# Performance work log

Hardware: AMD Instinct MI355X
Metric: run time of the kernel (lower is better)

The kernel has to match this reference:

```python
import jax, jax.numpy as jnp
import numpy as np

NHEAD, HD, ITERS = 8, 32, 6


def _layernorm(x, g, b, eps=1e-5):
    mu = jnp.mean(x, axis=-1, keepdims=True)
    var = jnp.mean((x - mu) ** 2, axis=-1, keepdims=True)
    return g * (x - mu) / jnp.sqrt(var + eps) + b


def _msa1(x, ax, WQ, bQ, WK, bK, WV, bV, WO, bO):
    # ring (sliding-window, size 3) attention + relay node as 4th key/value
    B, L, H = x.shape
    q = (x @ WQ + bQ).reshape(B, L, NHEAD, HD)
    k = (x @ WK + bK).reshape(B, L, NHEAD, HD)
    ak = (ax @ WK + bK).reshape(B, 1, NHEAD, 1, HD)   # relay key
    av = (ax @ WV + bV).reshape(B, 1, NHEAD, 1, HD)   # relay value
    padk = jnp.pad(k, ((0, 0), (1, 1), (0, 0), (0, 0)))
    wins = jnp.stack([padk[:, t:L + t] for t in range(3)], axis=3)  # [B,L,nh,3,hd]
    ak_b = jnp.broadcast_to(ak, (B, L, NHEAD, 1, HD))
    av_b = jnp.broadcast_to(av, (B, L, NHEAD, 1, HD))
    keys = jnp.concatenate([ak_b, wins], axis=3)   # [B,L,nh,4,hd]
    # NOTE: faithful to source bug: window VALUES come from k (pad_v = F.pad(k,...))
    vals = jnp.concatenate([av_b, wins], axis=3)
    scores = jnp.einsum('blnd,blnkd->blnk', q, keys) / np.sqrt(HD).astype(np.float32)
    alphas = jax.nn.softmax(scores, axis=-1)
    att = jnp.einsum('blnk,blnkd->blnd', alphas, vals).reshape(B, L, NHEAD * HD)
    return att @ WO + bO


def _msa2(x, y, WQ, bQ, WK, bK, WV, bV, WO, bO):
    # relay attends over [relay; nodes]; mask arg is ignored in the original
    B, L1, H = y.shape
    q = (x @ WQ + bQ).reshape(B, NHEAD, HD)
    k = (y @ WK + bK).reshape(B, L1, NHEAD, HD)
    v = (y @ WV + bV).reshape(B, L1, NHEAD, HD)
    scores = jnp.einsum('bnd,blnd->bnl', q, k) / np.sqrt(HD).astype(np.float32)
    alphas = jax.nn.softmax(scores, axis=-1)
    att = jnp.einsum('bnl,blnd->bnd', alphas, v).reshape(B, NHEAD * HD)
    return att @ WO + bO


def setup_inputs() -> dict:
    key = jax.random.key(0)
    ks = jax.random.split(key, 32)
    B, L, H, V, E, I = 32, 512, 256, 32000, 300, 6

    def rn(k, shape, s=0.05):
        return jax.random.normal(k, shape, jnp.float32) * s

    inp = {
        'data': jax.random.randint(ks[0], (B, L), 0, V),
        'emb': rn(ks[1], (V, E), 0.1),
        'emb_fc_W': rn(ks[2], (E, H)),
        'emb_fc_b': jnp.zeros((H,), jnp.float32),
        'pos_emb': rn(ks[3], (1000, H), 0.02),
        'ln_g': jnp.ones((I, H), jnp.float32),
        'ln_b': jnp.zeros((I, H), jnp.float32),
    }
    names = ['r_WQ', 'r_WK', 'r_WV', 'r_WO', 's_WQ', 's_WK', 's_WV', 's_WO']
    for j, n in enumerate(names):
        inp[n] = rn(ks[4 + j], (I, H, H))
        inp[n.replace('W', 'b')] = rn(ks[12 + j], (I, H), 0.01)
    return inp


def reference(data, emb, emb_fc_W, emb_fc_b, pos_emb, ln_g, ln_b,
              r_WQ, r_bQ, r_WK, r_bK, r_WV, r_bV, r_WO, r_bO,
              s_WQ, s_bQ, s_WK, s_bK, s_WV, s_bV, s_WO, s_bO):
    B, L = data.shape
    mask = (data == 1)
    e = emb[data]                                  # [B,L,nemb]
    P = pos_emb[:L][None]                          # [1,L,H]
    x0 = e @ emb_fc_W + emb_fc_b + P               # [B,L,H]
    nodes = x0
    relay = jnp.mean(x0, axis=1)                   # [B,H]
    for i in range(ITERS):
        ax = relay
        n_ln = _layernorm(nodes, ln_g[i], ln_b[i])
        nodes = nodes + jax.nn.leaky_relu(
            _msa1(n_ln, ax, r_WQ[i], r_bQ[i], r_WK[i], r_bK[i],
                  r_WV[i], r_bV[i], r_WO[i], r_bO[i]))
        y = jnp.concatenate([relay[:, None, :], nodes], axis=1)
        relay = jax.nn.leaky_relu(
            _msa2(relay, y, s_WQ[i], s_bQ[i], s_WK[i], s_bK[i],
                  s_WV[i], s_bV[i], s_WO[i], s_bO[i]))
        nodes = jnp.where(mask[:, :, None], 0.0, nodes)
    rep = 0.5 * jnp.max(nodes, axis=1) + 0.5 * relay
    return rep
```

## Files before the change

kernel.cpp:

```cpp
#include <hip/hip_runtime.h>
#include <stdint.h>

typedef __bf16 bf16x8 __attribute__((ext_vector_type(8)));
typedef unsigned short ushort8 __attribute__((ext_vector_type(8)));
typedef float floatx4 __attribute__((ext_vector_type(4)));

__device__ __forceinline__ unsigned short f2b(float f) {
    unsigned int u = __builtin_bit_cast(unsigned int, f);
    u += 0x7fffu + ((u >> 16) & 1u);
    return (unsigned short)(u >> 16);
}
__device__ __forceinline__ float b2f(unsigned short u) {
    union { unsigned int i; float f; } x; x.i = ((unsigned int)u) << 16; return x.f;
}
__device__ __forceinline__ void gl_lds16(const unsigned short* g, unsigned short* l) {
    __builtin_amdgcn_global_load_lds(
        (const __attribute__((address_space(1))) unsigned int*)g,
        (__attribute__((address_space(3))) unsigned int*)l, 16, 0, 0);
}

#define SCALE_QK 0.17677669529663687f

__global__ void transpose_many(const float* __restrict__ w0,
                               const float* __restrict__ w1,
                               const float* __restrict__ w2,
                               const float* __restrict__ w3,
                               const float* __restrict__ w4,
                               unsigned short* __restrict__ out) {
    int m = blockIdx.y;
    int fam = m / 6, it = m % 6;
    const float* src =
        (fam == 0 ? w0 : fam == 1 ? w1 : fam == 2 ? w2 : fam == 3 ? w3 : w4) + it * 65536;
    int e = blockIdx.x * 256 + threadIdx.x;
    int n = e >> 8, k = e & 255;
    out[(size_t)(it * 5 + fam) * 65536 + e] = f2b(src[k * 256 + n]);
}

__global__ void transpose_emb(const float* __restrict__ W,
                              unsigned short* __restrict__ out) {
    int e = blockIdx.x * 256 + threadIdx.x;
    int n = e / 320, k = e % 320;
    out[e] = (k < 300) ? f2b(W[k * 256 + n]) : (unsigned short)0;
}

__global__ void gather_emb(const int* __restrict__ data,
                           const float* __restrict__ emb,
                           unsigned short* __restrict__ apad) {
    int row = blockIdx.x;
    int tok = data[row];
    const float* er = emb + (size_t)tok * 300;
    for (int c = threadIdx.x; c < 320; c += 256)
        apad[(size_t)row * 320 + c] = (c < 300) ? f2b(er[c]) : (unsigned short)0;
}

template <int EPI, int KDIM>
__global__ __launch_bounds__(256) void gemm_k(const unsigned short* __restrict__ A,
                                              const unsigned short* __restrict__ Bt,
                                              const float* __restrict__ bias0,
                                              const float* __restrict__ bias1,
                                              float* __restrict__ outF,
                                              unsigned short* __restrict__ outB0,
                                              unsigned short* __restrict__ outB1,
                                              const float* __restrict__ pos,
                                              const int* __restrict__ dmask,
                                              int applyMask) {
    constexpr int G = KDIM / 8;
    __shared__ unsigned short Asm[64 * KDIM];
    __shared__ unsigned short Bsm[64 * KDIM];
    const int tid = threadIdx.x;
    const int wave = tid >> 6, lane = tid & 63;
    const int wm = (wave >> 1) * 32, wn = (wave & 1) * 32;
    const int quad = lane >> 4, l16 = lane & 15;
    const int rowBase = blockIdx.x * 64, colBase = blockIdx.y * 64;

    {
        const unsigned short* gbA = A + (size_t)(rowBase + wave * 16) * KDIM;
        const unsigned short* gbB = Bt + (size_t)(colBase + wave * 16) * KDIM;
        unsigned short* lbA = Asm + wave * 16 * KDIM;
        unsigned short* lbB = Bsm + wave * 16 * KDIM;
#pragma unroll
        for (int c = 0; c < G / 4; c++) {
            int gi = c * 64 + lane;
            int rl = gi / G, sl = gi - rl * G;
            int sg = sl ^ (rl & 7);
            gl_lds16(gbA + rl * KDIM + sg * 8, lbA + gi * 8);
            gl_lds16(gbB + rl * KDIM + sg * 8, lbB + gi * 8);
        }
    }
    __syncthreads();

    floatx4 acc[2][2] = {};
    const int mr0 = wm + l16, mr1 = wm + 16 + l16;
    const int nr0 = wn + l16, nr1 = wn + 16 + l16;
#pragma unroll
    for (int ks = 0; ks < KDIM / 32; ks++) {
        int g = ks * 4 + quad;
        bf16x8 af0 = __builtin_bit_cast(bf16x8, *(const ushort8*)&Asm[mr0 * KDIM + ((g ^ (mr0 & 7)) * 8)]);
        bf16x8 af1 = __builtin_bit_cast(bf16x8, *(const ushort8*)&Asm[mr1 * KDIM + ((g ^ (mr1 & 7)) * 8)]);
        bf16x8 bf0 = __builtin_bit_cast(bf16x8, *(const ushort8*)&Bsm[nr0 * KDIM + ((g ^ (nr0 & 7)) * 8)]);
        bf16x8 bf1 = __builtin_bit_cast(bf16x8, *(const ushort8*)&Bsm[nr1 * KDIM + ((g ^ (nr1 & 7)) * 8)]);
        acc[0][0] = __builtin_amdgcn_mfma_f32_16x16x32_bf16(af0, bf0, acc[0][0], 0, 0, 0);
        acc[0][1] = __builtin_amdgcn_mfma_f32_16x16x32_bf16(af0, bf1, acc[0][1], 0, 0, 0);
        acc[1][0] = __builtin_amdgcn_mfma_f32_16x16x32_bf16(af1, bf0, acc[1][0], 0, 0, 0);
        acc[1][1] = __builtin_amdgcn_mfma_f32_16x16x32_bf16(af1, bf1, acc[1][1], 0, 0, 0);
    }
    const int group = colBase >> 8;
    const float* bias = (EPI == 0 && group) ? bias1 : bias0;
    unsigned short* obf = (EPI == 0 && group) ? outB1 : outB0;
#pragma unroll
    for (int tm = 0; tm < 2; tm++) {
#pragma unroll
        for (int tn = 0; tn < 2; tn++) {
            int col = colBase + wn + tn * 16 + l16;
            int lc = col & 255;
            float bv = bias[lc];
#pragma unroll
            for (int r = 0; r < 4; r++) {
                int row = rowBase + wm + tm * 16 + quad * 4 + r;
                float c = acc[tm][tn][r] + bv;
                size_t o = (size_t)row * 256 + lc;
                if (EPI == 0) {
                    obf[o] = f2b(c);
                } else if (EPI == 1) {
                    float v = c > 0.f ? c : 0.01f * c;
                    float base = outF[o];
                    if (applyMask && dmask[row] == 1) base = 0.f;
                    float rr = base + v;
                    outF[o] = rr;
                    outB0[o] = f2b(rr);
                } else {
                    outF[o] = c + pos[(row & 511) * 256 + lc];
                }
            }
        }
    }
}

__global__ void mean_part(const float* __restrict__ nodes, float* __restrict__ part) {
    int b = blockIdx.x, c = blockIdx.y, h = threadIdx.x;
    const float* p = nodes + ((size_t)b * 512 + c * 32) * 256 + h;
    float s = 0.f;
    for (int l = 0; l < 32; l++) s += p[l * 256];
    part[(b * 16 + c) * 256 + h] = s;
}
__global__ void mean_comb(const float* __restrict__ part, float* __restrict__ relay) {
    int b = blockIdx.x, h = threadIdx.x;
    float s = 0.f;
    for (int c = 0; c < 16; c++) s += part[(b * 16 + c) * 256 + h];
    relay[b * 256 + h] = s * (1.f / 512.f);
}

__global__ __launch_bounds__(256) void ln_k(const float* __restrict__ nodes,
                                            const float* __restrict__ g,
                                            const float* __restrict__ bb,
                                            unsigned short* __restrict__ out,
                                            const int* __restrict__ dmask,
                                            int applyMask) {
    __shared__ float red[8];
    int row = blockIdx.x, t = threadIdx.x;
    int wv = t >> 6, ln_ = t & 63;
    float x = nodes[(size_t)row * 256 + t];
    if (applyMask && dmask[row] == 1) x = 0.f;
    float s = x;
#pragma unroll
    for (int o = 32; o; o >>= 1) s += __shfl_xor(s, o);
    if (ln_ == 0) red[wv] = s;
    __syncthreads();
    float mu = (red[0] + red[1] + red[2] + red[3]) * (1.f / 256.f);
    float d = x - mu;
    float v = d * d;
#pragma unroll
    for (int o = 32; o; o >>= 1) v += __shfl_xor(v, o);
    if (ln_ == 0) red[4 + wv] = v;
    __syncthreads();
    float var = (red[4] + red[5] + red[6] + red[7]) * (1.f / 256.f);
    float inv = rsqrtf(var + 1e-5f);
    out[(size_t)row * 256 + t] = f2b(g[t] * d * inv + bb[t]);
}

__global__ void relay5(const float* __restrict__ relay,
                       const float* __restrict__ rWK, const float* __restrict__ rbK,
                       const float* __restrict__ rWV, const float* __restrict__ rbV,
                       const float* __restrict__ sWQ, const float* __restrict__ sbQ,
                       const float* __restrict__ sWK, const float* __restrict__ sbK,
                       const float* __restrict__ sWV, const float* __restrict__ sbV,
                       float* __restrict__ AK, float* __restrict__ AV,
                       float* __restrict__ Q2, float* __restrict__ RK2, float* __restrict__ RV2) {
    __shared__ float r[256];
    int b = blockIdx.x, fam = blockIdx.y, t = threadIdx.x;
    r[t] = relay[b * 256 + t];
    __syncthreads();
    const float* W; const float* bi; float* o;
    switch (fam) {
        case 0: W = rWK; bi = rbK; o = AK; break;
        case 1: W = rWV; bi = rbV; o = AV; break;
        case 2: W = sWQ; bi = sbQ; o = Q2; break;
        case 3: W = sWK; bi = sbK; o = RK2; break;
        default: W = sWV; bi = sbV; o = RV2; break;
    }
    float s = 0.f;
    for (int e = 0; e < 256; e++) s += r[e] * W[e * 256 + t];
    o[b * 256 + t] = s + bi[t];
}

__global__ __launch_bounds__(256) void attn1_k(const unsigned short* __restrict__ q,
                                               const unsigned short* __restrict__ k,
                                               const float* __restrict__ ak,
                                               const float* __restrict__ av,
                                               unsigned short* __restrict__ att) {
    int tid = threadIdx.x;
    int row = blockIdx.x * 4 + (tid >> 6);
    int b = row >> 9, l = row & 511;
    int t = tid & 63;
    size_t o = (size_t)row * 256 + t * 4;
    ushort4 z4; z4.x = z4.y = z4.z = z4.w = 0;
    ushort4 q4 = *(const ushort4*)(q + o);
    ushort4 k04 = *(const ushort4*)(k + o);
    ushort4 km4 = (l > 0) ? *(const ushort4*)(k + o - 256) : z4;
    ushort4 kp4 = (l < 511) ? *(const ushort4*)(k + o + 256) : z4;
    float4 akv = *(const float4*)(ak + b * 256 + t * 4);
    float4 avv = *(const float4*)(av + b * 256 + t * 4);
    float qv0 = b2f(q4.x), qv1 = b2f(q4.y), qv2 = b2f(q4.z), qv3 = b2f(q4.w);
    float k00 = b2f(k04.x), k01 = b2f(k04.y), k02 = b2f(k04.z), k03 = b2f(k04.w);
    float km0 = b2f(km4.x), km1 = b2f(km4.y), km2 = b2f(km4.z), km3 = b2f(km4.w);
    float kp0 = b2f(kp4.x), kp1 = b2f(kp4.y), kp2 = b2f(kp4.z), kp3 = b2f(kp4.w);
    float s0 = qv0 * akv.x + qv1 * akv.y + qv2 * akv.z + qv3 * akv.w;
    float s1 = qv0 * km0 + qv1 * km1 + qv2 * km2 + qv3 * km3;
    float s2 = qv0 * k00 + qv1 * k01 + qv2 * k02 + qv3 * k03;
    float s3 = qv0 * kp0 + qv1 * kp1 + qv2 * kp2 + qv3 * kp3;
#pragma unroll
    for (int off = 4; off; off >>= 1) {
        s0 += __shfl_xor(s0, off);
        s1 += __shfl_xor(s1, off);
        s2 += __shfl_xor(s2, off);
        s3 += __shfl_xor(s3, off);
    }
    s0 *= SCALE_QK; s1 *= SCALE_QK; s2 *= SCALE_QK; s3 *= SCALE_QK;
    float m = fmaxf(fmaxf(s0, s1), fmaxf(s2, s3));
    float e0 = __expf(s0 - m), e1 = __expf(s1 - m), e2 = __expf(s2 - m), e3 = __expf(s3 - m);
    float iZ = 1.f / (e0 + e1 + e2 + e3);
    ushort4 r4;
    r4.x = f2b((e0 * avv.x + e1 * km0 + e2 * k00 + e3 * kp0) * iZ);
    r4.y = f2b((e0 * avv.y + e1 * km1 + e2 * k01 + e3 * kp1) * iZ);
    r4.z = f2b((e0 * avv.z + e1 * km2 + e2 * k02 + e3 * kp2) * iZ);
    r4.w = f2b((e0 * avv.w + e1 * km3 + e2 * k03 + e3 * kp3) * iZ);
    *(ushort4*)(att + o) = r4;
}

__global__ __launch_bounds__(256) void attn2_k(const float* __restrict__ q2,
                                               const unsigned short* __restrict__ k2,
                                               const unsigned short* __restrict__ v2,
                                               const float* __restrict__ rk2,
                                               const float* __restrict__ rv2,
                                               float* __restrict__ att2) {
    __shared__ float sc[513];
    __shared__ float qs[32];
    __shared__ float red[16];
    __shared__ float red2[256];
    int bn = blockIdx.x;
    int b = bn >> 3, n = bn & 7;
    int t = threadIdx.x;
    if (t < 32) qs[t] = q2[b * 256 + n * 32 + t];
    __syncthreads();
    float lmax = -1e30f;
    for (int li = t; li < 513; li += 256) {
        float d = 0.f;
        if (li == 0) {
            const float* kr = rk2 + b * 256 + n * 32;
#pragma unroll 8
            for (int j = 0; j < 32; j++) d += qs[j] * kr[j];
        } else {
            const unsigned short* kr = k2 + ((size_t)(b * 512 + li - 1) * 256 + n * 32);
#pragma unroll 8
            for (int j = 0; j < 32; j++) d += qs[j] * b2f(kr[j]);
        }
        d *= SCALE_QK;
        sc[li] = d;
        lmax = fmaxf(lmax, d);
    }
#pragma unroll
    for (int o = 32; o; o >>= 1) lmax = fmaxf(lmax, __shfl_xor(lmax, o));
    if ((t & 63) == 0) red[t >> 6] = lmax;
    __syncthreads();
    float m = fmaxf(fmaxf(red[0], red[1]), fmaxf(red[2], red[3]));
    float lsum = 0.f;
    for (int li = t; li < 513; li += 256) {
        float e = __expf(sc[li] - m);
        sc[li] = e;
        lsum += e;
    }
#pragma unroll
    for (int o = 32; o; o >>= 1) lsum += __shfl_xor(lsum, o);
    if ((t & 63) == 0) red[8 + (t >> 6)] = lsum;
    __syncthreads();
    float Z = red[8] + red[9] + red[10] + red[11];
    int d_ = t & 31, g_ = t >> 5;
    float acc = 0.f;
    for (int li = g_; li < 513; li += 8) {
        if (li == 0) {
            acc += sc[0] * rv2[b * 256 + n * 32 + d_];
        } else {
            acc += sc[li] * b2f(v2[(size_t)(b * 512 + li - 1) * 256 + n * 32 + d_]);
        }
    }
    red2[t] = acc;
    __syncthreads();
    if (t < 32) {
        float s = 0.f;
        for (int g = 0; g < 8; g++) s += red2[g * 32 + t];
        att2[b * 256 + n * 32 + t] = s / Z;
    }
}

__global__ void relay_out2(const float* __restrict__ att2,
                           const float* __restrict__ WO, const float* __restrict__ bO,
                           float* __restrict__ relay) {
    __shared__ float r[256];
    int b = blockIdx.x, t = threadIdx.x;
    r[t] = att2[b * 256 + t];
    __syncthreads();
    float s = 0.f;
    for (int e = 0; e < 256; e++) s += r[e] * WO[e * 256 + t];
    s += bO[t];
    relay[b * 256 + t] = s > 0.f ? s : 0.01f * s;
}

__global__ void rep_part(const float* __restrict__ nodes, const int* __restrict__ dmask,
                         float* __restrict__ part) {
    int b = blockIdx.x, c = blockIdx.y, h = threadIdx.x;
    const float* p = nodes + ((size_t)b * 512 + c * 32) * 256 + h;
    const int* dd = dmask + b * 512 + c * 32;
    float m = -1e30f;
    for (int l = 0; l < 32; l++) {
        float v = (dd[l] == 1) ? 0.f : p[l * 256];
        m = fmaxf(m, v);
    }
    part[(b * 16 + c) * 256 + h] = m;
}
__global__ void rep_comb(const float* __restrict__ part, const float* __restrict__ relay,
                         float* __restrict__ out) {
    int b = blockIdx.x, h = threadIdx.x;
    float m = -1e30f;
    for (int c = 0; c < 16; c++) m = fmaxf(m, part[(b * 16 + c) * 256 + h]);
    out[b * 256 + h] = 0.5f * m + 0.5f * relay[b * 256 + h];
}

extern "C" void kernel_launch(void* const* d_in, const int* in_sizes, int n_in,
                              void* d_out, int out_size, void* d_ws, size_t ws_size,
                              hipStream_t stream) {
    const int* data = (const int*)d_in[0];
    const float* emb = (const float*)d_in[1];
    const float* emb_fc_W = (const float*)d_in[2];
    const float* emb_fc_b = (const float*)d_in[3];
    const float* pos_emb = (const float*)d_in[4];
    const float* ln_g = (const float*)d_in[5];
    const float* ln_b = (const float*)d_in[6];
    const float* r_WQ = (const float*)d_in[7];
    const float* r_bQ = (const float*)d_in[8];
    const float* r_WK = (const float*)d_in[9];
    const float* r_bK = (const float*)d_in[10];
    const float* r_WV = (const float*)d_in[11];
    const float* r_bV = (const float*)d_in[12];
    const float* r_WO = (const float*)d_in[13];
    const float* r_bO = (const float*)d_in[14];
    const float* s_WQ = (const float*)d_in[15];
    const float* s_bQ = (const float*)d_in[16];
    const float* s_WK = (const float*)d_in[17];
    const float* s_bK = (const float*)d_in[18];
    const float* s_WV = (const float*)d_in[19];
    const float* s_bV = (const float*)d_in[20];
    const float* s_WO = (const float*)d_in[21];
    const float* s_bO = (const float*)d_in[22];

    char* w = (char*)d_ws;
    size_t off = 0;
    auto alloc = [&](size_t bytes) -> char* {
        char* p = w + off;
        off += (bytes + 255) & ~(size_t)255;
        return p;
    };
    float* RELAY = (float*)alloc(8192 * 4);
    float* AK = (float*)alloc(8192 * 4);
    float* AV = (float*)alloc(8192 * 4);
    float* Q2 = (float*)alloc(8192 * 4);
    float* RK2 = (float*)alloc(8192 * 4);
    float* RV2 = (float*)alloc(8192 * 4);
    float* ATT2 = (float*)alloc(8192 * 4);
    float* PART = (float*)alloc((size_t)32 * 16 * 256 * 4);
    unsigned short* WTE = (unsigned short*)alloc((size_t)256 * 320 * 2);
    unsigned short* WT = (unsigned short*)alloc((size_t)30 * 65536 * 2);
    float* NODES = (float*)alloc((size_t)16384 * 256 * 4);
    unsigned short* NLN = (unsigned short*)alloc((size_t)16384 * 256 * 2);
    unsigned short* Qb = (unsigned short*)alloc((size_t)16384 * 256 * 2);
    unsigned short* Kb16 = (unsigned short*)alloc((size_t)16384 * 256 * 2);
    unsigned short* NBF = (unsigned short*)alloc((size_t)16384 * 320 * 2);
    unsigned short* AEMB = NBF;
    unsigned short* ATT = NLN;
    unsigned short* K2b = Qb;
    unsigned short* V2b = Kb16;

    transpose_many<<<dim3(256, 30), 256, 0, stream>>>(r_WQ, r_WK, r_WO, s_WK, s_WV, WT);
    transpose_emb<<<320, 256, 0, stream>>>(emb_fc_W, WTE);
    gather_emb<<<16384, 256, 0, stream>>>(data, emb, AEMB);
    gemm_k<2, 320><<<dim3(256, 4), 256, 0, stream>>>(AEMB, WTE, emb_fc_b, nullptr,
                                                     NODES, nullptr, nullptr, pos_emb, nullptr, 0);
    mean_part<<<dim3(32, 16), 256, 0, stream>>>(NODES, PART);
    mean_comb<<<32, 256, 0, stream>>>(PART, RELAY);

    for (int i = 0; i < 6; i++) {
        const unsigned short* wQK = WT + (size_t)(i * 5 + 0) * 65536;
        const unsigned short* wO = WT + (size_t)(i * 5 + 2) * 65536;
        const unsigned short* wKV2 = WT + (size_t)(i * 5 + 3) * 65536;

        ln_k<<<16384, 256, 0, stream>>>(NODES, ln_g + i * 256, ln_b + i * 256, NLN, data, i > 0);
        gemm_k<0, 256><<<dim3(256, 8), 256, 0, stream>>>(NLN, wQK, r_bQ + i * 256, r_bK + i * 256,
                                                         nullptr, Qb, Kb16, nullptr, nullptr, 0);
        relay5<<<dim3(32, 5), 256, 0, stream>>>(RELAY,
                                                r_WK + (size_t)i * 65536, r_bK + i * 256,
                                                r_WV + (size_t)i * 65536, r_bV + i * 256,
                                                s_WQ + (size_t)i * 65536, s_bQ + i * 256,
                                                s_WK + (size_t)i * 65536, s_bK + i * 256,
                                                s_WV + (size_t)i * 65536, s_bV + i * 256,
                                                AK, AV, Q2, RK2, RV2);
        attn1_k<<<4096, 256, 0, stream>>>(Qb, Kb16, AK, AV, ATT);
        gemm_k<1, 256><<<dim3(256, 4), 256, 0, stream>>>(ATT, wO, r_bO + i * 256, nullptr,
                                                         NODES, NBF, nullptr, nullptr, data, i > 0);
        gemm_k<0, 256><<<dim3(256, 8), 256, 0, stream>>>(NBF, wKV2, s_bK + i * 256, s_bV + i * 256,
                                                         nullptr, K2b, V2b, nullptr, nullptr, 0);
        attn2_k<<<256, 256, 0, stream>>>(Q2, K2b, V2b, RK2, RV2, ATT2);
        relay_out2<<<32, 256, 0, stream>>>(ATT2, s_WO + (size_t)i * 65536, s_bO + i * 256, RELAY);
    }
    rep_part<<<dim3(32, 16), 256, 0, stream>>>(NODES, data, PART);
    rep_comb<<<32, 256, 0, stream>>>(PART, RELAY, (float*)d_out);
}
```

Measured before the change: 852.3 us.

## Fuse layernorm into QK GEMM and ring attention into WO GEMM

Layernorm is now computed inside the QK projection GEMM while filling the A tile in shared memory. Ring attention is computed inside the output projection GEMM, so the separate LN and attention kernels and their intermediate bf16 buffers go away. This removes two launches per iteration and the write and re-read of the intermediates. In exchange, each row's LN is recomputed per column block (8x) and the attention per column block (4x). The A-tile fill becomes synchronous compute instead of async loads. The variance now uses the E[x^2]-mu^2 formula.

```diff
diff --git a/kernel.cpp b/kernel.cpp
--- a/kernel.cpp
+++ b/kernel.cpp
@@ -61,9 +61,7 @@
                                               float* __restrict__ outF,
                                               unsigned short* __restrict__ outB0,
                                               unsigned short* __restrict__ outB1,
-                                              const float* __restrict__ pos,
-                                              const int* __restrict__ dmask,
-                                              int applyMask) {
+                                              const float* __restrict__ pos) {
     constexpr int G = KDIM / 8;
     __shared__ unsigned short Asm[64 * KDIM];
     __shared__ unsigned short Bsm[64 * KDIM];
@@ -72,7 +70,6 @@
     const int wm = (wave >> 1) * 32, wn = (wave & 1) * 32;
     const int quad = lane >> 4, l16 = lane & 15;
     const int rowBase = blockIdx.x * 64, colBase = blockIdx.y * 64;
-
     {
         const unsigned short* gbA = A + (size_t)(rowBase + wave * 16) * KDIM;
         const unsigned short* gbB = Bt + (size_t)(colBase + wave * 16) * KDIM;
@@ -121,16 +118,208 @@
                 size_t o = (size_t)row * 256 + lc;
                 if (EPI == 0) {
                     obf[o] = f2b(c);
-                } else if (EPI == 1) {
-                    float v = c > 0.f ? c : 0.01f * c;
-                    float base = outF[o];
-                    if (applyMask && dmask[row] == 1) base = 0.f;
-                    float rr = base + v;
-                    outF[o] = rr;
-                    outB0[o] = f2b(rr);
                 } else {
                     outF[o] = c + pos[(row & 511) * 256 + lc];
                 }
+            }
+        }
+    }
+}
+
+__global__ __launch_bounds__(256) void lnqk_gemm(const float* __restrict__ nodes,
+                                                 const float* __restrict__ lg,
+                                                 const float* __restrict__ lb,
+                                                 const unsigned short* __restrict__ Bt,
+                                                 const float* __restrict__ bQ,
+                                                 const float* __restrict__ bK,
+                                                 unsigned short* __restrict__ Qb,
+                                                 unsigned short* __restrict__ Kb,
+                                                 const int* __restrict__ dmask,
+                                                 int applyMask) {
+    __shared__ unsigned short Asm[64 * 256];
+    __shared__ unsigned short Bsm[64 * 256];
+    const int tid = threadIdx.x;
+    const int wave = tid >> 6, lane = tid & 63;
+    const int rowBase = blockIdx.x * 64, colBase = blockIdx.y * 64;
+    {
+        const unsigned short* gb = Bt + (size_t)(colBase + wave * 16) * 256;
+        unsigned short* lb_ = Bsm + wave * 16 * 256;
+#pragma unroll
+        for (int c = 0; c < 8; c++) {
+            int gi = c * 64 + lane;
+            int rl = gi >> 5, sl = gi & 31;
+            int sg = sl ^ (rl & 7);
+            gl_lds16(gb + rl * 256 + sg * 8, lb_ + gi * 8);
+        }
+    }
+    {
+        const int cb = lane * 4;
+        float4 gv = *(const float4*)(lg + cb);
+        float4 bv = *(const float4*)(lb + cb);
+        for (int i = 0; i < 16; i++) {
+            int row = rowBase + wave * 16 + i;
+            float4 x = *(const float4*)(nodes + (size_t)row * 256 + cb);
+            if (applyMask && dmask[row] == 1) { x.x = 0.f; x.y = 0.f; x.z = 0.f; x.w = 0.f; }
+            float s = x.x + x.y + x.z + x.w;
+            float qq = x.x * x.x + x.y * x.y + x.z * x.z + x.w * x.w;
+#pragma unroll
+            for (int o = 32; o; o >>= 1) { s += __shfl_xor(s, o); qq += __shfl_xor(qq, o); }
+            float mu = s * (1.f / 256.f);
+            float var = qq * (1.f / 256.f) - mu * mu;
+            float inv = rsqrtf(fmaxf(var, 0.f) + 1e-5f);
+            ushort4 r4;
+            r4.x = f2b(gv.x * (x.x - mu) * inv + bv.x);
+            r4.y = f2b(gv.y * (x.y - mu) * inv + bv.y);
+            r4.z = f2b(gv.z * (x.z - mu) * inv + bv.z);
+            r4.w = f2b(gv.w * (x.w - mu) * inv + bv.w);
+            int r = wave * 16 + i;
+            int slot = (lane >> 1) ^ (r & 7);
+            *(ushort4*)&Asm[r * 256 + slot * 8 + (lane & 1) * 4] = r4;
+        }
+    }
+    __syncthreads();
+
+    floatx4 acc[2][2] = {};
+    const int wm = (wave >> 1) * 32, wn = (wave & 1) * 32;
+    const int quad = lane >> 4, l16 = lane & 15;
+    const int mr0 = wm + l16, mr1 = wm + 16 + l16;
+    const int nr0 = wn + l16, nr1 = wn + 16 + l16;
+#pragma unroll
+    for (int ks = 0; ks < 8; ks++) {
+        int g = ks * 4 + quad;
+        bf16x8 af0 = __builtin_bit_cast(bf16x8, *(const ushort8*)&Asm[mr0 * 256 + ((g ^ (mr0 & 7)) * 8)]);
+        bf16x8 af1 = __builtin_bit_cast(bf16x8, *(const ushort8*)&Asm[mr1 * 256 + ((g ^ (mr1 & 7)) * 8)]);
+        bf16x8 bf0 = __builtin_bit_cast(bf16x8, *(const ushort8*)&Bsm[nr0 * 256 + ((g ^ (nr0 & 7)) * 8)]);
+        bf16x8 bf1 = __builtin_bit_cast(bf16x8, *(const ushort8*)&Bsm[nr1 * 256 + ((g ^ (nr1 & 7)) * 8)]);
+        acc[0][0] = __builtin_amdgcn_mfma_f32_16x16x32_bf16(af0, bf0, acc[0][0], 0, 0, 0);
+        acc[0][1] = __builtin_amdgcn_mfma_f32_16x16x32_bf16(af0, bf1, acc[0][1], 0, 0, 0);
+        acc[1][0] = __builtin_amdgcn_mfma_f32_16x16x32_bf16(af1, bf0, acc[1][0], 0, 0, 0);
+        acc[1][1] = __builtin_amdgcn_mfma_f32_16x16x32_bf16(af1, bf1, acc[1][1], 0, 0, 0);
+    }
+    const int group = colBase >> 8;
+    const float* bias = group ? bK : bQ;
+    unsigned short* obf = group ? Kb : Qb;
+#pragma unroll
+    for (int tm = 0; tm < 2; tm++) {
+#pragma unroll
+        for (int tn = 0; tn < 2; tn++) {
+            int col = colBase + wn + tn * 16 + l16;
+            int lc = col & 255;
+            float bv = bias[lc];
+#pragma unroll
+            for (int r = 0; r < 4; r++) {
+                int row = rowBase + wm + tm * 16 + quad * 4 + r;
+                obf[(size_t)row * 256 + lc] = f2b(acc[tm][tn][r] + bv);
+            }
+        }
+    }
+}
+
+__global__ __launch_bounds__(256) void att_wo_gemm(const unsigned short* __restrict__ q,
+                                                   const unsigned short* __restrict__ k,
+                                                   const float* __restrict__ ak,
+                                                   const float* __restrict__ av,
+                                                   const unsigned short* __restrict__ Bt,
+                                                   const float* __restrict__ bO,
+                                                   float* __restrict__ NODES,
+                                                   unsigned short* __restrict__ NBF,
+                                                   const int* __restrict__ dmask,
+                                                   int applyMask) {
+    __shared__ unsigned short Asm[64 * 256];
+    __shared__ unsigned short Bsm[64 * 256];
+    const int tid = threadIdx.x;
+    const int wave = tid >> 6, lane = tid & 63;
+    const int rowBase = blockIdx.x * 64, colBase = blockIdx.y * 64;
+    {
+        const unsigned short* gb = Bt + (size_t)(colBase + wave * 16) * 256;
+        unsigned short* lb_ = Bsm + wave * 16 * 256;
+#pragma unroll
+        for (int c = 0; c < 8; c++) {
+            int gi = c * 64 + lane;
+            int rl = gi >> 5, sl = gi & 31;
+            int sg = sl ^ (rl & 7);
+            gl_lds16(gb + rl * 256 + sg * 8, lb_ + gi * 8);
+        }
+    }
+    {
+        const int bb = rowBase >> 9;
+        const int cb = lane * 4;
+        float4 akv = *(const float4*)(ak + bb * 256 + cb);
+        float4 avv = *(const float4*)(av + bb * 256 + cb);
+        ushort4 z4; z4.x = z4.y = z4.z = z4.w = 0;
+        for (int i = 0; i < 16; i++) {
+            int row = rowBase + wave * 16 + i;
+            int l = row & 511;
+            size_t o = (size_t)row * 256 + cb;
+            ushort4 q4 = *(const ushort4*)(q + o);
+            ushort4 k04 = *(const ushort4*)(k + o);
+            ushort4 km4 = (l > 0) ? *(const ushort4*)(k + o - 256) : z4;
+            ushort4 kp4 = (l < 511) ? *(const ushort4*)(k + o + 256) : z4;
+            float qv0 = b2f(q4.x), qv1 = b2f(q4.y), qv2 = b2f(q4.z), qv3 = b2f(q4.w);
+            float k00 = b2f(k04.x), k01 = b2f(k04.y), k02 = b2f(k04.z), k03 = b2f(k04.w);
+            float km0 = b2f(km4.x), km1 = b2f(km4.y), km2 = b2f(km4.z), km3 = b2f(km4.w);
+            float kp0 = b2f(kp4.x), kp1 = b2f(kp4.y), kp2 = b2f(kp4.z), kp3 = b2f(kp4.w);
+            float s0 = qv0 * akv.x + qv1 * akv.y + qv2 * akv.z + qv3 * akv.w;
+            float s1 = qv0 * km0 + qv1 * km1 + qv2 * km2 + qv3 * km3;
+            float s2 = qv0 * k00 + qv1 * k01 + qv2 * k02 + qv3 * k03;
+            float s3 = qv0 * kp0 + qv1 * kp1 + qv2 * kp2 + qv3 * kp3;
+#pragma unroll
+            for (int off = 4; off; off >>= 1) {
+                s0 += __shfl_xor(s0, off);
+                s1 += __shfl_xor(s1, off);
+                s2 += __shfl_xor(s2, off);
+                s3 += __shfl_xor(s3, off);
+            }
+            s0 *= SCALE_QK; s1 *= SCALE_QK; s2 *= SCALE_QK; s3 *= SCALE_QK;
+            float m = fmaxf(fmaxf(s0, s1), fmaxf(s2, s3));
+            float e0 = __expf(s0 - m), e1 = __expf(s1 - m), e2 = __expf(s2 - m), e3 = __expf(s3 - m);
+            float iZ = 1.f / (e0 + e1 + e2 + e3);
+            ushort4 r4;
+            r4.x = f2b((e0 * avv.x + e1 * km0 + e2 * k00 + e3 * kp0) * iZ);
+            r4.y = f2b((e0 * avv.y + e1 * km1 + e2 * k01 + e3 * kp1) * iZ);
+            r4.z = f2b((e0 * avv.z + e1 * km2 + e2 * k02 + e3 * kp2) * iZ);
+            r4.w = f2b((e0 * avv.w + e1 * km3 + e2 * k03 + e3 * kp3) * iZ);
+            int r = wave * 16 + i;
+            int slot = (lane >> 1) ^ (r & 7);
+            *(ushort4*)&Asm[r * 256 + slot * 8 + (lane & 1) * 4] = r4;
+        }
+    }
+    __syncthreads();
+
+    floatx4 acc[2][2] = {};
+    const int wm = (wave >> 1) * 32, wn = (wave & 1) * 32;
+    const int quad = lane >> 4, l16 = lane & 15;
+    const int mr0 = wm + l16, mr1 = wm + 16 + l16;
+    const int nr0 = wn + l16, nr1 = wn + 16 + l16;
+#pragma unroll
+    for (int ks = 0; ks < 8; ks++) {
+        int g = ks * 4 + quad;
+        bf16x8 af0 = __builtin_bit_cast(bf16x8, *(const ushort8*)&Asm[mr0 * 256 + ((g ^ (mr0 & 7)) * 8)]);
+        bf16x8 af1 = __builtin_bit_cast(bf16x8, *(const ushort8*)&Asm[mr1 * 256 + ((g ^ (mr1 & 7)) * 8)]);
+        bf16x8 bf0 = __builtin_bit_cast(bf16x8, *(const ushort8*)&Bsm[nr0 * 256 + ((g ^ (nr0 & 7)) * 8)]);
+        bf16x8 bf1 = __builtin_bit_cast(bf16x8, *(const ushort8*)&Bsm[nr1 * 256 + ((g ^ (nr1 & 7)) * 8)]);
+        acc[0][0] = __builtin_amdgcn_mfma_f32_16x16x32_bf16(af0, bf0, acc[0][0], 0, 0, 0);
+        acc[0][1] = __builtin_amdgcn_mfma_f32_16x16x32_bf16(af0, bf1, acc[0][1], 0, 0, 0);
+        acc[1][0] = __builtin_amdgcn_mfma_f32_16x16x32_bf16(af1, bf0, acc[1][0], 0, 0, 0);
+        acc[1][1] = __builtin_amdgcn_mfma_f32_16x16x32_bf16(af1, bf1, acc[1][1], 0, 0, 0);
+    }
+#pragma unroll
+    for (int tm = 0; tm < 2; tm++) {
+#pragma unroll
+        for (int tn = 0; tn < 2; tn++) {
+            int col = colBase + wn + tn * 16 + l16;
+            float bv = bO[col];
+#pragma unroll
+            for (int r = 0; r < 4; r++) {
+                int row = rowBase + wm + tm * 16 + quad * 4 + r;
+                float c = acc[tm][tn][r] + bv;
+                float v = c > 0.f ? c : 0.01f * c;
+                size_t o = (size_t)row * 256 + col;
+                float base = NODES[o];
+                if (applyMask && dmask[row] == 1) base = 0.f;
+                float rr = base + v;
+                NODES[o] = rr;
+                NBF[o] = f2b(rr);
             }
         }
     }
@@ -148,34 +337,6 @@
     float s = 0.f;
     for (int c = 0; c < 16; c++) s += part[(b * 16 + c) * 256 + h];
     relay[b * 256 + h] = s * (1.f / 512.f);
-}
-
-__global__ __launch_bounds__(256) void ln_k(const float* __restrict__ nodes,
-                                            const float* __restrict__ g,
-                                            const float* __restrict__ bb,
-                                            unsigned short* __restrict__ out,
-                                            const int* __restrict__ dmask,
-                                            int applyMask) {
-    __shared__ float red[8];
-    int row = blockIdx.x, t = threadIdx.x;
-    int wv = t >> 6, ln_ = t & 63;
-    float x = nodes[(size_t)row * 256 + t];
-    if (applyMask && dmask[row] == 1) x = 0.f;
-    float s = x;
-#pragma unroll
-    for (int o = 32; o; o >>= 1) s += __shfl_xor(s, o);
-    if (ln_ == 0) red[wv] = s;
-    __syncthreads();
-    float mu = (red[0] + red[1] + red[2] + red[3]) * (1.f / 256.f);
-    float d = x - mu;
-    float v = d * d;
-#pragma unroll
-    for (int o = 32; o; o >>= 1) v += __shfl_xor(v, o);
-    if (ln_ == 0) red[4 + wv] = v;
-    __syncthreads();
-    float var = (red[4] + red[5] + red[6] + red[7]) * (1.f / 256.f);
-    float inv = rsqrtf(var + 1e-5f);
-    out[(size_t)row * 256 + t] = f2b(g[t] * d * inv + bb[t]);
 }
 
 __global__ void relay5(const float* __restrict__ relay,
@@ -201,50 +362,6 @@
     float s = 0.f;
     for (int e = 0; e < 256; e++) s += r[e] * W[e * 256 + t];
     o[b * 256 + t] = s + bi[t];
-}
-
-__global__ __launch_bounds__(256) void attn1_k(const unsigned short* __restrict__ q,
-                                               const unsigned short* __restrict__ k,
-                                               const float* __restrict__ ak,
-                                               const float* __restrict__ av,
-                                               unsigned short* __restrict__ att) {
-    int tid = threadIdx.x;
-    int row = blockIdx.x * 4 + (tid >> 6);
-    int b = row >> 9, l = row & 511;
-    int t = tid & 63;
-    size_t o = (size_t)row * 256 + t * 4;
-    ushort4 z4; z4.x = z4.y = z4.z = z4.w = 0;
-    ushort4 q4 = *(const ushort4*)(q + o);
-    ushort4 k04 = *(const ushort4*)(k + o);
-    ushort4 km4 = (l > 0) ? *(const ushort4*)(k + o - 256) : z4;
-    ushort4 kp4 = (l < 511) ? *(const ushort4*)(k + o + 256) : z4;
-    float4 akv = *(const float4*)(ak + b * 256 + t * 4);
-    float4 avv = *(const float4*)(av + b * 256 + t * 4);
-    float qv0 = b2f(q4.x), qv1 = b2f(q4.y), qv2 = b2f(q4.z), qv3 = b2f(q4.w);
-    float k00 = b2f(k04.x), k01 = b2f(k04.y), k02 = b2f(k04.z), k03 = b2f(k04.w);
-    float km0 = b2f(km4.x), km1 = b2f(km4.y), km2 = b2f(km4.z), km3 = b2f(km4.w);
-    float kp0 = b2f(kp4.x), kp1 = b2f(kp4.y), kp2 = b2f(kp4.z), kp3 = b2f(kp4.w);
-    float s0 = qv0 * akv.x + qv1 * akv.y + qv2 * akv.z + qv3 * akv.w;
-    float s1 = qv0 * km0 + qv1 * km1 + qv2 * km2 + qv3 * km3;
-    float s2 = qv0 * k00 + qv1 * k01 + qv2 * k02 + qv3 * k03;
-    float s3 = qv0 * kp0 + qv1 * kp1 + qv2 * kp2 + qv3 * kp3;
-#pragma unroll
-    for (int off = 4; off; off >>= 1) {
-        s0 += __shfl_xor(s0, off);
-        s1 += __shfl_xor(s1, off);
-        s2 += __shfl_xor(s2, off);
-        s3 += __shfl_xor(s3, off);
-    }
-    s0 *= SCALE_QK; s1 *= SCALE_QK; s2 *= SCALE_QK; s3 *= SCALE_QK;
-    float m = fmaxf(fmaxf(s0, s1), fmaxf(s2, s3));
-    float e0 = __expf(s0 - m), e1 = __expf(s1 - m), e2 = __expf(s2 - m), e3 = __expf(s3 - m);
-    float iZ = 1.f / (e0 + e1 + e2 + e3);
-    ushort4 r4;
-    r4.x = f2b((e0 * avv.x + e1 * km0 + e2 * k00 + e3 * kp0) * iZ);
-    r4.y = f2b((e0 * avv.y + e1 * km1 + e2 * k01 + e3 * kp1) * iZ);
-    r4.z = f2b((e0 * avv.z + e1 * km2 + e2 * k02 + e3 * kp2) * iZ);
-    r4.w = f2b((e0 * avv.w + e1 * km3 + e2 * k03 + e3 * kp3) * iZ);
-    *(ushort4*)(att + o) = r4;
 }
 
 __global__ __launch_bounds__(256) void attn2_k(const float* __restrict__ q2,
@@ -390,12 +507,10 @@
     unsigned short* WTE = (unsigned short*)alloc((size_t)256 * 320 * 2);
     unsigned short* WT = (unsigned short*)alloc((size_t)30 * 65536 * 2);
     float* NODES = (float*)alloc((size_t)16384 * 256 * 4);
-    unsigned short* NLN = (unsigned short*)alloc((size_t)16384 * 256 * 2);
     unsigned short* Qb = (unsigned short*)alloc((size_t)16384 * 256 * 2);
     unsigned short* Kb16 = (unsigned short*)alloc((size_t)16384 * 256 * 2);
     unsigned short* NBF = (unsigned short*)alloc((size_t)16384 * 320 * 2);
     unsigned short* AEMB = NBF;
-    unsigned short* ATT = NLN;
     unsigned short* K2b = Qb;
     unsigned short* V2b = Kb16;
 
@@ -403,7 +518,7 @@
     transpose_emb<<<320, 256, 0, stream>>>(emb_fc_W, WTE);
     gather_emb<<<16384, 256, 0, stream>>>(data, emb, AEMB);
     gemm_k<2, 320><<<dim3(256, 4), 256, 0, stream>>>(AEMB, WTE, emb_fc_b, nullptr,
-                                                     NODES, nullptr, nullptr, pos_emb, nullptr, 0);
+                                                     NODES, nullptr, nullptr, pos_emb);
     mean_part<<<dim3(32, 16), 256, 0, stream>>>(NODES, PART);
     mean_comb<<<32, 256, 0, stream>>>(PART, RELAY);
 
@@ -412,9 +527,9 @@
         const unsigned short* wO = WT + (size_t)(i * 5 + 2) * 65536;
         const unsigned short* wKV2 = WT + (size_t)(i * 5 + 3) * 65536;
 
-        ln_k<<<16384, 256, 0, stream>>>(NODES, ln_g + i * 256, ln_b + i * 256, NLN, data, i > 0);
-        gemm_k<0, 256><<<dim3(256, 8), 256, 0, stream>>>(NLN, wQK, r_bQ + i * 256, r_bK + i * 256,
-                                                         nullptr, Qb, Kb16, nullptr, nullptr, 0);
+        lnqk_gemm<<<dim3(256, 8), 256, 0, stream>>>(NODES, ln_g + i * 256, ln_b + i * 256,
+                                                    wQK, r_bQ + i * 256, r_bK + i * 256,
+                                                    Qb, Kb16, data, i > 0);
         relay5<<<dim3(32, 5), 256, 0, stream>>>(RELAY,
                                                 r_WK + (size_t)i * 65536, r_bK + i * 256,
                                                 r_WV + (size_t)i * 65536, r_bV + i * 256,
@@ -422,11 +537,10 @@
                                                 s_WK + (size_t)i * 65536, s_bK + i * 256,
                                                 s_WV + (size_t)i * 65536, s_bV + i * 256,
                                                 AK, AV, Q2, RK2, RV2);
-        attn1_k<<<4096, 256, 0, stream>>>(Qb, Kb16, AK, AV, ATT);
-        gemm_k<1, 256><<<dim3(256, 4), 256, 0, stream>>>(ATT, wO, r_bO + i * 256, nullptr,
-                                                         NODES, NBF, nullptr, nullptr, data, i > 0);
+        att_wo_gemm<<<dim3(256, 4), 256, 0, stream>>>(Qb, Kb16, AK, AV, wO, r_bO + i * 256,
+                                                      NODES, NBF, data, i > 0);
         gemm_k<0, 256><<<dim3(256, 8), 256, 0, stream>>>(NBF, wKV2, s_bK + i * 256, s_bV + i * 256,
-                                                         nullptr, K2b, V2b, nullptr, nullptr, 0);
+                                                         nullptr, K2b, V2b, nullptr);
         attn2_k<<<256, 256, 0, stream>>>(Q2, K2b, V2b, RK2, RV2, ATT2);
         relay_out2<<<32, 256, 0, stream>>>(ATT2, s_WO + (size_t)i * 65536, s_bO + i * 256, RELAY);
     }
```

New measurement: 1.165 ms. 36.7% more time.
